# Performance work log

Hardware: AMD Instinct MI355X
Metric: run time of the kernel (lower is better)

Reference implementation:

```python
import jax, jax.numpy as jnp
import numpy as np


def _segsum(x):
    """Stable segment-sum. x: (..., l) -> (..., l, l) lower-triangular sums."""
    l = x.shape[-1]
    cs = jnp.cumsum(x, axis=-1)
    seg = cs[..., :, None] - cs[..., None, :]
    mask = jnp.tril(jnp.ones((l, l), dtype=bool))
    return jnp.where(mask, seg, -jnp.inf)


def setup_inputs() -> dict:
    key = jax.random.key(0)
    kx, ka, kb, kc = jax.random.split(key, 4)
    b, s, h, p, n = 4, 8192, 32, 64, 16
    X = jax.random.normal(kx, (b, s, h, p), dtype=jnp.float32)
    # negative A for realistic decaying SSM dynamics / numerical safety
    A = -jnp.abs(jax.random.normal(ka, (b, s, h), dtype=jnp.float32)) * 0.5
    B = jax.random.normal(kb, (b, s, h, n), dtype=jnp.float32)
    C = jax.random.normal(kc, (b, s, h, n), dtype=jnp.float32)
    return {"X": X, "A": A, "B": B, "C": C, "block_len": 64}


def reference(X, A, B, C, block_len):
    b, s, h, p = X.shape
    n = B.shape[-1]
    c = s // block_len
    l = block_len
    # chunk: (b, c, l, ...)
    Xb = X.reshape(b, c, l, h, p)
    Bb = B.reshape(b, c, l, h, n)
    Cb = C.reshape(b, c, l, h, n)
    Ab = A.reshape(b, c, l, h).transpose(0, 3, 1, 2)  # (b, h, c, l)
    A_cumsum = jnp.cumsum(Ab, axis=-1)                # (b, h, c, l)

    # 1) intra-chunk (diagonal) output
    L = jnp.exp(_segsum(Ab))                          # (b, h, c, l, l)
    Y_diag = jnp.einsum("bclhn,bcshn,bhcls,bcshp->bclhp", Cb, Bb, L, Xb)

    # 2) intra-chunk states (chunk-final state contribution)
    decay_states = jnp.exp(A_cumsum[..., -1:] - A_cumsum)   # (b, h, c, l)
    states = jnp.einsum("bclhn,bhcl,bclhp->bchpn", Bb, decay_states, Xb)

    # 3) inter-chunk recurrence (zero initial states)
    A_last = A_cumsum[..., -1]                        # (b, h, c)
    decay_chunk = jnp.exp(_segsum(jnp.pad(A_last, ((0, 0), (0, 0), (1, 0)))))  # (b,h,c+1,c+1)
    states = jnp.concatenate([jnp.zeros_like(states[:, :1]), states], axis=1)  # (b,c+1,h,p,n)
    new_states = jnp.einsum("bhzc,bchpn->bzhpn", decay_chunk, states)
    states = new_states[:, :-1]                       # states entering each chunk

    # 4) state -> output (off-diagonal)
    state_decay_out = jnp.exp(A_cumsum)               # (b, h, c, l)
    Y_off = jnp.einsum("bclhn,bchpn,bhcl->bclhp", Cb, states, state_decay_out)

    Y = (Y_diag + Y_off).reshape(b, s, h, p)
    return Y
```

## Files before the change

kernel.cpp:

```cpp
#include <hip/hip_runtime.h>

#define BB 4
#define SS 8192
#define HH 32
#define PP 64
#define NN 16
#define LL 64
#define CC 128
#define NCHAIN (BB * HH)
#define NCHT (NCHAIN * CC)

typedef __attribute__((ext_vector_type(8))) short bf16x8;
typedef __attribute__((ext_vector_type(4))) short bf16x4;
typedef __attribute__((ext_vector_type(4))) float f32x4;

__device__ inline short f2bf(float f) {
    unsigned u = __builtin_bit_cast(unsigned, f);
    u = (u + 0x7FFFu + ((u >> 16) & 1u)) >> 16;
    return (short)u;
}

__global__ __launch_bounds__(256) void k1_states(
    const float* __restrict__ X, const float* __restrict__ A,
    const float* __restrict__ B, float* __restrict__ states,
    float* __restrict__ alast_g)
{
    int blk = blockIdx.x;
    int h = blk & (HH - 1);
    int c = (blk >> 5) & (CC - 1);
    int b = blk >> 12;
    int tid = threadIdx.x;
    int w = tid >> 6, l = tid & 63, g = l >> 4, lr = l & 15;
    int chain = b * HH + h;

    __shared__ float Bs[LL][17];

    size_t row0 = (size_t)b * SS + (size_t)c * LL;
    const float* Xp = X + (row0 * HH + h) * PP;
    const float* Bp = B + (row0 * HH + h) * NN;
    const float* Ap = A + row0 * HH + h;

    float av = Ap[(size_t)l * HH];
    int r = tid >> 2, q = tid & 3;
    float4 br = *(const float4*)(Bp + (size_t)r * (HH * NN) + q * 4);
    float xr[16];
#pragma unroll
    for (int kt = 0; kt < 2; ++kt)
#pragma unroll
        for (int e = 0; e < 8; ++e)
            xr[kt * 8 + e] = Xp[(size_t)(kt * 32 + g * 8 + e) * (HH * PP) + 16 * w + lr];

    float x = av;
#pragma unroll
    for (int d = 1; d < 64; d <<= 1) {
        float t = __shfl_up(x, d, 64);
        if (l >= d) x += t;
    }
    float alast = __shfl(x, 63, 64);

    float wlr = __expf(alast - __shfl(x, r & 63, 64));
    Bs[r][q * 4 + 0] = br.x * wlr;
    Bs[r][q * 4 + 1] = br.y * wlr;
    Bs[r][q * 4 + 2] = br.z * wlr;
    Bs[r][q * 4 + 3] = br.w * wlr;
    __syncthreads();

    bf16x8 bt[2], xf[2];
#pragma unroll
    for (int kt = 0; kt < 2; ++kt)
#pragma unroll
        for (int e = 0; e < 8; ++e) {
            int row = kt * 32 + g * 8 + e;
            bt[kt][e] = f2bf(Bs[row][lr]);
            xf[kt][e] = f2bf(xr[kt * 8 + e]);
        }
    f32x4 st = __builtin_amdgcn_mfma_f32_16x16x32_bf16(bt[0], xf[0], (f32x4)0.f, 0, 0, 0);
    st = __builtin_amdgcn_mfma_f32_16x16x32_bf16(bt[1], xf[1], st, 0, 0, 0);

    float4 pv = {st[0], st[1], st[2], st[3]};
    *(float4*)(states + (size_t)(chain * CC + c) * (PP * NN) + (16 * w + lr) * NN + 4 * g) = pv;
    if (tid == 0) alast_g[chain * CC + c] = alast;
}

__global__ __launch_bounds__(256) void k2_scan(
    float* __restrict__ states, const float* __restrict__ alast_g)
{
    int chain = blockIdx.x >> 2;
    int t = ((blockIdx.x & 3) << 8) + threadIdx.x;
    __shared__ float eal[CC];
    if (threadIdx.x < CC)
        eal[threadIdx.x] = __expf(alast_g[chain * CC + threadIdx.x]);
    __syncthreads();

    float* base = states + (size_t)chain * CC * (PP * NN) + t;
    float P = 0.f;
    for (int c0 = 0; c0 < CC; c0 += 8) {
        float s[8], o[8];
#pragma unroll
        for (int u = 0; u < 8; ++u) s[u] = base[(size_t)(c0 + u) * (PP * NN)];
#pragma unroll
        for (int u = 0; u < 8; ++u) { o[u] = P; P = eal[c0 + u] * P + s[u]; }
#pragma unroll
        for (int u = 0; u < 8; ++u) base[(size_t)(c0 + u) * (PP * NN)] = o[u];
    }
}

__global__ __launch_bounds__(256) void k3_y(
    const float* __restrict__ X, const float* __restrict__ A,
    const float* __restrict__ Bm, const float* __restrict__ Cm,
    const float* __restrict__ pin, float* __restrict__ Y)
{
    int blk = blockIdx.x;
    int h = blk & (HH - 1);
    int c = (blk >> 5) & (CC - 1);
    int b = blk >> 12;
    int tid = threadIdx.x;
    int w = tid >> 6, l = tid & 63, g = l >> 4, lr = l & 15;
    int chain = b * HH + h;

    __shared__ short XTF[8 * 64 * 8];
    __shared__ short ScF[8 * 64 * 8];
    __shared__ short BsF[4 * 64 * 8];
    __shared__ short PF[4 * 64 * 8];

    size_t row0 = (size_t)b * SS + (size_t)c * LL;
    const float* Xp = X + (row0 * HH + h) * PP;
    const float* Bp = Bm + (row0 * HH + h) * NN;
    const float* Cp = Cm + (row0 * HH + h) * NN;
    const float* Ap = A + row0 * HH + h;
    float* Yp = Y + (row0 * HH + h) * PP;

    float av = Ap[(size_t)l * HH];
    int r = tid >> 2, q = tid & 3;
    float4 br = *(const float4*)(Bp + (size_t)r * (HH * NN) + q * 4);
    float4 cr0 = {0,0,0,0}, cr1 = {0,0,0,0};
    if (g < 2) {
        const float* crp = Cp + (size_t)(16 * w + lr) * (HH * NN) + g * 8;
        cr0 = *(const float4*)crp;
        cr1 = *(const float4*)(crp + 4);
    }
    float4 pinv = *(const float4*)(pin + (size_t)(chain * CC + c) * (PP * NN) + (16 * w + lr) * NN + 4 * g);
    float xr[16];
#pragma unroll
    for (int si = 0; si < 2; ++si) {
        int k0 = si * 32 + g * 8;
#pragma unroll
        for (int e = 0; e < 8; ++e)
            xr[si * 8 + e] = Xp[(size_t)(k0 + e) * (HH * PP) + 16 * w + lr];
    }

    float x = av;
#pragma unroll
    for (int d = 1; d < 64; d <<= 1) {
        float t = __shfl_up(x, d, 64);
        if (l >= d) x += t;
    }
    float cs_i[4], ei[4];
    int ib = 16 * w + 4 * g;
#pragma unroll
    for (int rr = 0; rr < 4; ++rr) {
        cs_i[rr] = __shfl(x, ib + rr, 64);
        ei[rr] = __expf(cs_i[rr]);
    }

    ((bf16x8*)ScF)[tid] = (bf16x8)0;
    ((bf16x8*)ScF)[tid + 256] = (bf16x8)0;
    if (tid < 128)
        ((bf16x8*)PF)[(tid >> 5) * 64 + 32 + (tid & 31)] = (bf16x8)0;
    {
        int fl = (r & 15) + 16 * (q >> 1);
        int jt = r >> 4;
        bf16x4 bb = { f2bf(br.x), f2bf(br.y), f2bf(br.z), f2bf(br.w) };
        ((bf16x4*)BsF)[(jt * 64 + fl) * 2 + (q & 1)] = bb;
        int zt = tid >> 6, zu = (tid >> 1) & 31, zv = tid & 1;
        ((bf16x4*)BsF)[(zt * 64 + 32 + zu) * 2 + zv] = (bf16x4)0;
    }
    {
        float P4[4] = {pinv.x, pinv.y, pinv.z, pinv.w};
#pragma unroll
        for (int rr = 0; rr < 4; ++rr) {
            int n = 4 * g + rr;
            PF[(w * 64 + (n >> 3) * 16 + lr) * 8 + (n & 7)] = f2bf(P4[rr]);
        }
    }
    bf16x8 caw = (bf16x8)0;
    if (g < 2) {
        caw[0] = f2bf(cr0.x); caw[1] = f2bf(cr0.y);
        caw[2] = f2bf(cr0.z); caw[3] = f2bf(cr0.w);
        caw[4] = f2bf(cr1.x); caw[5] = f2bf(cr1.y);
        caw[6] = f2bf(cr1.z); caw[7] = f2bf(cr1.w);
    }
    __syncthreads();

    f32x4 acc[4];
#pragma unroll
    for (int pt = 0; pt < 4; ++pt) {
        bf16x8 pfv = ((bf16x8*)PF)[pt * 64 + l];
        acc[pt] = __builtin_amdgcn_mfma_f32_16x16x32_bf16(caw, pfv, (f32x4)0.f, 0, 0, 0);
    }
#pragma unroll
    for (int pt = 0; pt < 4; ++pt)
#pragma unroll
        for (int rr = 0; rr < 4; ++rr) acc[pt][rr] *= ei[rr];

    for (int jt = 0; jt <= w; ++jt) {
        bf16x8 bw = ((bf16x8*)BsF)[jt * 64 + l];
        f32x4 sr = __builtin_amdgcn_mfma_f32_16x16x32_bf16(caw, bw, (f32x4)0.f, 0, 0, 0);
        int j = jt * 16 + lr;
        float csj = __shfl(x, j, 64);
        int kt2 = j >> 5;
        int flb = 16 * ((j >> 3) & 3);
#pragma unroll
        for (int rr = 0; rr < 4; ++rr) {
            int i15 = g * 4 + rr;
            int i = 16 * w + i15;
            float v = (j <= i) ? sr[rr] * __expf(cs_i[rr] - csj) : 0.f;
            ScF[((w * 2 + kt2) * 64 + i15 + flb) * 8 + (j & 7)] = f2bf(v);
        }
    }

#pragma unroll
    for (int si = 0; si < 2; ++si) {
        bf16x8 xb;
#pragma unroll
        for (int e = 0; e < 8; ++e) xb[e] = f2bf(xr[si * 8 + e]);
        ((bf16x8*)XTF)[tid + si * 256] = xb;
    }
    __syncthreads();

    int kts = (w >= 2) ? 2 : 1;
    for (int kt = 0; kt < kts; ++kt) {
        bf16x8 af = ((bf16x8*)ScF)[(w * 2 + kt) * 64 + l];
#pragma unroll
        for (int pt = 0; pt < 4; ++pt) {
            bf16x8 xf = ((bf16x8*)XTF)[(kt * 4 + pt) * 64 + l];
            acc[pt] = __builtin_amdgcn_mfma_f32_16x16x32_bf16(af, xf, acc[pt], 0, 0, 0);
        }
    }

#pragma unroll
    for (int pt = 0; pt < 4; ++pt)
#pragma unroll
        for (int rr = 0; rr < 4; ++rr)
            Yp[(size_t)(16 * w + 4 * g + rr) * (HH * PP) + pt * 16 + lr] = acc[pt][rr];
}

extern "C" void kernel_launch(void* const* d_in, const int* in_sizes, int n_in,
                              void* d_out, int out_size, void* d_ws, size_t ws_size,
                              hipStream_t stream)
{
    const float* X = (const float*)d_in[0];
    const float* A = (const float*)d_in[1];
    const float* B = (const float*)d_in[2];
    const float* C = (const float*)d_in[3];
    float* Y = (float*)d_out;

    float* states = (float*)d_ws;
    float* alast  = states + (size_t)NCHT * (PP * NN);

    dim3 blk(256);
    k1_states<<<dim3(NCHT), blk, 0, stream>>>(X, A, B, states, alast);
    k2_scan<<<dim3(NCHAIN * 4), blk, 0, stream>>>(states, alast);
    k3_y<<<dim3(NCHT), blk, 0, stream>>>(X, A, B, C, states, Y);
}
```

Before: 276.3 us.

## Persistent double-buffered kernels, bf16 states, and cached bf16 X fragments

The state and Y kernels become persistent: each block handles several chunks and prefetches the next chunk's inputs into registers and double-buffered shared memory while computing the current one. Chunk states are stored and scanned as bf16 instead of fp32, which halves that traffic. When the workspace is large enough, k1 also writes bf16-converted X fragments that k3 reads instead of re-reading and converting fp32 X. This trades extra workspace writes and lower state precision for less traffic and launch overhead.

Result: faster. 262.1 us (-5.2%).

```diff
diff --git a/kernel.cpp b/kernel.cpp
--- a/kernel.cpp
+++ b/kernel.cpp
@@ -9,9 +9,11 @@
 #define CC 128
 #define NCHAIN (BB * HH)
 #define NCHT (NCHAIN * CC)
+#define ITERS 8
+#define GRID1 (NCHT / ITERS)
 
 typedef __attribute__((ext_vector_type(8))) short bf16x8;
-typedef __attribute__((ext_vector_type(4))) short bf16x4;
+typedef __attribute__((ext_vector_type(4))) short s16x4;
 typedef __attribute__((ext_vector_type(4))) float f32x4;
 
 __device__ inline short f2bf(float f) {
@@ -19,11 +21,237 @@
     u = (u + 0x7FFFu + ((u >> 16) & 1u)) >> 16;
     return (short)u;
 }
+__device__ inline float bf2f(short s) {
+    unsigned u = ((unsigned)(unsigned short)s) << 16;
+    return __builtin_bit_cast(float, u);
+}
+__device__ inline float wscan(float v, int l) {
+    float x = v;
+#pragma unroll
+    for (int d = 1; d < 64; d <<= 1) {
+        float t = __shfl_up(x, d, 64);
+        if (l >= d) x += t;
+    }
+    return x;
+}
 
 __global__ __launch_bounds__(256) void k1_states(
     const float* __restrict__ X, const float* __restrict__ A,
-    const float* __restrict__ B, float* __restrict__ states,
-    float* __restrict__ alast_g)
+    const float* __restrict__ B, short* __restrict__ states,
+    float* __restrict__ alast_g, short* __restrict__ xtf, int do_xtf)
+{
+    int tid = threadIdx.x;
+    int w = tid >> 6, l = tid & 63, g = l >> 4, lr = l & 15;
+    int r = tid >> 2, q4 = tid & 3;
+    int bid = blockIdx.x;
+
+    __shared__ float Bs[2][LL][17];
+
+    float xrA[16], xrB[16];
+    float4 br; float av;
+
+#define K1_LOADS(gc_, xr_) { \
+    int h_ = (gc_) & 31, c_ = ((gc_) >> 5) & 127, b_ = (gc_) >> 12; \
+    size_t row0_ = (size_t)b_ * SS + (size_t)c_ * LL; \
+    const float* Xp_ = X + (row0_ * HH + h_) * PP; \
+    av = (A + row0_ * HH + h_)[(size_t)l * HH]; \
+    br = *(const float4*)(B + (row0_ * HH + h_) * NN + (size_t)r * (HH * NN) + q4 * 4); \
+    _Pragma("unroll") for (int kt_ = 0; kt_ < 2; ++kt_) \
+    _Pragma("unroll") for (int e_ = 0; e_ < 8; ++e_) \
+        xr_[kt_ * 8 + e_] = Xp_[(size_t)(kt_ * 32 + g * 8 + e_) * (HH * PP) + 16 * w + lr]; }
+
+#define K1_STAGE(qd_, gc_) { \
+    float x_ = wscan(av, l); \
+    float alast_ = __shfl(x_, 63, 64); \
+    float wlr_ = __expf(alast_ - __shfl(x_, r, 64)); \
+    Bs[qd_][r][q4 * 4 + 0] = br.x * wlr_; \
+    Bs[qd_][r][q4 * 4 + 1] = br.y * wlr_; \
+    Bs[qd_][r][q4 * 4 + 2] = br.z * wlr_; \
+    Bs[qd_][r][q4 * 4 + 3] = br.w * wlr_; \
+    if (tid == 0) { \
+        int h_ = (gc_) & 31, c_ = ((gc_) >> 5) & 127, b_ = (gc_) >> 12; \
+        alast_g[(b_ * HH + h_) * CC + c_] = alast_; } }
+
+#define K1_COMPUTE(qd_, xr_, gc_) { \
+    int h_ = (gc_) & 31, c_ = ((gc_) >> 5) & 127, b_ = (gc_) >> 12; \
+    size_t cc_ = (size_t)((b_ * HH + h_) * CC + c_); \
+    bf16x8 bt0_, bt1_, xf0_, xf1_; \
+    _Pragma("unroll") for (int e_ = 0; e_ < 8; ++e_) { \
+        bt0_[e_] = f2bf(Bs[qd_][g * 8 + e_][lr]); \
+        bt1_[e_] = f2bf(Bs[qd_][32 + g * 8 + e_][lr]); \
+        xf0_[e_] = f2bf(xr_[e_]); xf1_[e_] = f2bf(xr_[8 + e_]); } \
+    f32x4 st_ = __builtin_amdgcn_mfma_f32_16x16x32_bf16(bt0_, xf0_, (f32x4)0.f, 0, 0, 0); \
+    st_ = __builtin_amdgcn_mfma_f32_16x16x32_bf16(bt1_, xf1_, st_, 0, 0, 0); \
+    s16x4 sp_ = { f2bf(st_[0]), f2bf(st_[1]), f2bf(st_[2]), f2bf(st_[3]) }; \
+    *(s16x4*)(states + (cc_ << 10) + ((16 * w + lr) << 4) + (g << 2)) = sp_; \
+    if (do_xtf) { \
+        short* xd_ = xtf + (cc_ << 12); \
+        ((bf16x8*)xd_)[tid] = xf0_; \
+        ((bf16x8*)xd_)[tid + 256] = xf1_; } }
+
+    K1_LOADS(bid, xrA)
+    K1_STAGE(0, bid)
+    __syncthreads();
+#pragma unroll
+    for (int t = 0; t < ITERS; ++t) {
+        int gc_c = bid + t * GRID1;
+        int gc_n = bid + (t + 1) * GRID1;
+        if (t + 1 < ITERS) {
+            if (t & 1) { K1_LOADS(gc_n, xrA) } else { K1_LOADS(gc_n, xrB) }
+        }
+        if (t & 1) { K1_COMPUTE(t & 1, xrB, gc_c) } else { K1_COMPUTE(t & 1, xrA, gc_c) }
+        if (t + 1 < ITERS) { K1_STAGE((t & 1) ^ 1, gc_n) }
+        __syncthreads();
+    }
+#undef K1_LOADS
+#undef K1_STAGE
+#undef K1_COMPUTE
+}
+
+__global__ __launch_bounds__(256) void k2_scan(
+    short* __restrict__ states, const float* __restrict__ alast_g)
+{
+    int chain = blockIdx.x >> 2;
+    int t = ((blockIdx.x & 3) << 8) + threadIdx.x;
+    __shared__ float eal[CC];
+    if (threadIdx.x < CC)
+        eal[threadIdx.x] = __expf(alast_g[chain * CC + threadIdx.x]);
+    __syncthreads();
+
+    short* base = states + ((size_t)chain * CC << 10) + t;
+    float P = 0.f;
+    for (int c0 = 0; c0 < CC; c0 += 8) {
+        short s[8];
+#pragma unroll
+        for (int u = 0; u < 8; ++u) s[u] = base[(size_t)(c0 + u) << 10];
+#pragma unroll
+        for (int u = 0; u < 8; ++u) {
+            float o = P;
+            P = eal[c0 + u] * P + bf2f(s[u]);
+            base[(size_t)(c0 + u) << 10] = f2bf(o);
+        }
+    }
+}
+
+__global__ __launch_bounds__(256) void k3_big(
+    const float* __restrict__ A, const float* __restrict__ Bm,
+    const float* __restrict__ Cm, const short* __restrict__ pin,
+    const short* __restrict__ xtf, float* __restrict__ Y)
+{
+    int tid = threadIdx.x;
+    int w = tid >> 6, l = tid & 63, g = l >> 4, lr = l & 15;
+    int r = tid >> 2, q4 = tid & 3;
+    int bid = blockIdx.x;
+
+    __shared__ short XTF[2][8 * 64 * 8];
+    __shared__ short BsF[2][4 * 64 * 8];
+    __shared__ short PF[2][4 * 64 * 8];
+    __shared__ short ScF[8 * 64 * 8];
+
+    ((bf16x8*)ScF)[w * 128 + l] = (bf16x8)0;
+    ((bf16x8*)ScF)[w * 128 + 64 + l] = (bf16x8)0;
+    if (tid < 128) {
+        ((bf16x8*)PF[0])[(tid >> 5) * 64 + 32 + (tid & 31)] = (bf16x8)0;
+        ((bf16x8*)PF[1])[(tid >> 5) * 64 + 32 + (tid & 31)] = (bf16x8)0;
+    }
+    {
+        int zt = tid >> 6, zu = (tid >> 1) & 31, zv = tid & 1;
+        ((s16x4*)BsF[0])[(zt * 64 + 32 + zu) * 2 + zv] = (s16x4)0;
+        ((s16x4*)BsF[1])[(zt * 64 + 32 + zu) * 2 + zv] = (s16x4)0;
+    }
+
+    bf16x8 xv0, xv1, caw_c, caw_n;
+    float4 br, cr0 = {0,0,0,0}, cr1 = {0,0,0,0};
+    s16x4 pinb; float av;
+    float x_c, x_n;
+
+#define K3_LOADS(gc_) { \
+    int h_ = (gc_) & 31, c_ = ((gc_) >> 5) & 127, b_ = (gc_) >> 12; \
+    size_t row0_ = (size_t)b_ * SS + (size_t)c_ * LL; \
+    size_t cc_ = (size_t)((b_ * HH + h_) * CC + c_); \
+    const short* xs_ = xtf + (cc_ << 12); \
+    xv0 = ((const bf16x8*)xs_)[tid]; \
+    xv1 = ((const bf16x8*)xs_)[tid + 256]; \
+    av = (A + row0_ * HH + h_)[(size_t)l * HH]; \
+    br = *(const float4*)(Bm + (row0_ * HH + h_) * NN + (size_t)r * (HH * NN) + q4 * 4); \
+    if (g < 2) { \
+        const float* cp_ = Cm + (row0_ * HH + h_) * NN + (size_t)(16 * w + lr) * (HH * NN) + g * 8; \
+        cr0 = *(const float4*)cp_; cr1 = *(const float4*)(cp_ + 4); } \
+    pinb = *(const s16x4*)(pin + (cc_ << 10) + ((16 * w + lr) << 4) + (g << 2)); }
+
+#define K3_STAGE(qd_) { \
+    x_n = wscan(av, l); \
+    ((bf16x8*)XTF[qd_])[tid] = xv0; \
+    ((bf16x8*)XTF[qd_])[tid + 256] = xv1; \
+    int fl_ = (r & 15) + 16 * (q4 >> 1); \
+    int jt_ = r >> 4; \
+    s16x4 bb_ = { f2bf(br.x), f2bf(br.y), f2bf(br.z), f2bf(br.w) }; \
+    ((s16x4*)BsF[qd_])[(jt_ * 64 + fl_) * 2 + (q4 & 1)] = bb_; \
+    ((s16x4*)PF[qd_])[(w * 64 + (g >> 1) * 16 + lr) * 2 + (g & 1)] = pinb; \
+    caw_n = (bf16x8)0; \
+    if (g < 2) { \
+        caw_n[0] = f2bf(cr0.x); caw_n[1] = f2bf(cr0.y); caw_n[2] = f2bf(cr0.z); caw_n[3] = f2bf(cr0.w); \
+        caw_n[4] = f2bf(cr1.x); caw_n[5] = f2bf(cr1.y); caw_n[6] = f2bf(cr1.z); caw_n[7] = f2bf(cr1.w); } }
+
+#define K3_COMPUTE(qd_, gc_) { \
+    int h_ = (gc_) & 31, c_ = ((gc_) >> 5) & 127, b_ = (gc_) >> 12; \
+    size_t row0_ = (size_t)b_ * SS + (size_t)c_ * LL; \
+    float* Yp_ = Y + (row0_ * HH + h_) * PP; \
+    float cs_i_[4], ei_[4]; \
+    int ib_ = 16 * w + 4 * g; \
+    _Pragma("unroll") for (int rr_ = 0; rr_ < 4; ++rr_) { \
+        cs_i_[rr_] = __shfl(x_c, ib_ + rr_, 64); ei_[rr_] = __expf(cs_i_[rr_]); } \
+    f32x4 acc_[4]; \
+    _Pragma("unroll") for (int pt_ = 0; pt_ < 4; ++pt_) { \
+        bf16x8 pfv_ = ((bf16x8*)PF[qd_])[pt_ * 64 + l]; \
+        acc_[pt_] = __builtin_amdgcn_mfma_f32_16x16x32_bf16(caw_c, pfv_, (f32x4)0.f, 0, 0, 0); } \
+    _Pragma("unroll") for (int pt_ = 0; pt_ < 4; ++pt_) \
+    _Pragma("unroll") for (int rr_ = 0; rr_ < 4; ++rr_) acc_[pt_][rr_] *= ei_[rr_]; \
+    for (int jt_ = 0; jt_ <= w; ++jt_) { \
+        bf16x8 bw_ = ((bf16x8*)BsF[qd_])[jt_ * 64 + l]; \
+        f32x4 sr_ = __builtin_amdgcn_mfma_f32_16x16x32_bf16(caw_c, bw_, (f32x4)0.f, 0, 0, 0); \
+        int j_ = jt_ * 16 + lr; \
+        float csj_ = __shfl(x_c, j_, 64); \
+        int kt2_ = j_ >> 5; \
+        int flb_ = 16 * ((j_ >> 3) & 3); \
+        _Pragma("unroll") for (int rr_ = 0; rr_ < 4; ++rr_) { \
+            int i15_ = g * 4 + rr_; \
+            int i_ = 16 * w + i15_; \
+            float v_ = (j_ <= i_) ? sr_[rr_] * __expf(cs_i_[rr_] - csj_) : 0.f; \
+            ScF[((w * 2 + kt2_) * 64 + i15_ + flb_) * 8 + (j_ & 7)] = f2bf(v_); } } \
+    int kts_ = (w >= 2) ? 2 : 1; \
+    for (int kt_ = 0; kt_ < kts_; ++kt_) { \
+        bf16x8 af_ = ((bf16x8*)ScF)[(w * 2 + kt_) * 64 + l]; \
+        _Pragma("unroll") for (int pt_ = 0; pt_ < 4; ++pt_) { \
+            bf16x8 xf_ = ((bf16x8*)XTF[qd_])[(kt_ * 4 + pt_) * 64 + l]; \
+            acc_[pt_] = __builtin_amdgcn_mfma_f32_16x16x32_bf16(af_, xf_, acc_[pt_], 0, 0, 0); } } \
+    _Pragma("unroll") for (int pt_ = 0; pt_ < 4; ++pt_) \
+    _Pragma("unroll") for (int rr_ = 0; rr_ < 4; ++rr_) \
+        Yp_[(size_t)(16 * w + 4 * g + rr_) * (HH * PP) + pt_ * 16 + lr] = acc_[pt_][rr_]; }
+
+    K3_LOADS(bid)
+    K3_STAGE(0)
+    x_c = x_n; caw_c = caw_n;
+    __syncthreads();
+#pragma unroll
+    for (int t = 0; t < ITERS; ++t) {
+        if (t + 1 < ITERS) { K3_LOADS(bid + (t + 1) * GRID1) }
+        K3_COMPUTE(t & 1, bid + t * GRID1)
+        if (t + 1 < ITERS) {
+            K3_STAGE((t + 1) & 1)
+            x_c = x_n; caw_c = caw_n;
+        }
+        __syncthreads();
+    }
+#undef K3_LOADS
+#undef K3_STAGE
+#undef K3_COMPUTE
+}
+
+__global__ __launch_bounds__(256) void k3_small(
+    const float* __restrict__ X, const float* __restrict__ A,
+    const float* __restrict__ Bm, const float* __restrict__ Cm,
+    const short* __restrict__ pin, float* __restrict__ Y)
 {
     int blk = blockIdx.x;
     int h = blk & (HH - 1);
@@ -32,91 +260,7 @@
     int tid = threadIdx.x;
     int w = tid >> 6, l = tid & 63, g = l >> 4, lr = l & 15;
     int chain = b * HH + h;
-
-    __shared__ float Bs[LL][17];
-
-    size_t row0 = (size_t)b * SS + (size_t)c * LL;
-    const float* Xp = X + (row0 * HH + h) * PP;
-    const float* Bp = B + (row0 * HH + h) * NN;
-    const float* Ap = A + row0 * HH + h;
-
-    float av = Ap[(size_t)l * HH];
     int r = tid >> 2, q = tid & 3;
-    float4 br = *(const float4*)(Bp + (size_t)r * (HH * NN) + q * 4);
-    float xr[16];
-#pragma unroll
-    for (int kt = 0; kt < 2; ++kt)
-#pragma unroll
-        for (int e = 0; e < 8; ++e)
-            xr[kt * 8 + e] = Xp[(size_t)(kt * 32 + g * 8 + e) * (HH * PP) + 16 * w + lr];
-
-    float x = av;
-#pragma unroll
-    for (int d = 1; d < 64; d <<= 1) {
-        float t = __shfl_up(x, d, 64);
-        if (l >= d) x += t;
-    }
-    float alast = __shfl(x, 63, 64);
-
-    float wlr = __expf(alast - __shfl(x, r & 63, 64));
-    Bs[r][q * 4 + 0] = br.x * wlr;
-    Bs[r][q * 4 + 1] = br.y * wlr;
-    Bs[r][q * 4 + 2] = br.z * wlr;
-    Bs[r][q * 4 + 3] = br.w * wlr;
-    __syncthreads();
-
-    bf16x8 bt[2], xf[2];
-#pragma unroll
-    for (int kt = 0; kt < 2; ++kt)
-#pragma unroll
-        for (int e = 0; e < 8; ++e) {
-            int row = kt * 32 + g * 8 + e;
-            bt[kt][e] = f2bf(Bs[row][lr]);
-            xf[kt][e] = f2bf(xr[kt * 8 + e]);
-        }
-    f32x4 st = __builtin_amdgcn_mfma_f32_16x16x32_bf16(bt[0], xf[0], (f32x4)0.f, 0, 0, 0);
-    st = __builtin_amdgcn_mfma_f32_16x16x32_bf16(bt[1], xf[1], st, 0, 0, 0);
-
-    float4 pv = {st[0], st[1], st[2], st[3]};
-    *(float4*)(states + (size_t)(chain * CC + c) * (PP * NN) + (16 * w + lr) * NN + 4 * g) = pv;
-    if (tid == 0) alast_g[chain * CC + c] = alast;
-}
-
-__global__ __launch_bounds__(256) void k2_scan(
-    float* __restrict__ states, const float* __restrict__ alast_g)
-{
-    int chain = blockIdx.x >> 2;
-    int t = ((blockIdx.x & 3) << 8) + threadIdx.x;
-    __shared__ float eal[CC];
-    if (threadIdx.x < CC)
-        eal[threadIdx.x] = __expf(alast_g[chain * CC + threadIdx.x]);
-    __syncthreads();
-
-    float* base = states + (size_t)chain * CC * (PP * NN) + t;
-    float P = 0.f;
-    for (int c0 = 0; c0 < CC; c0 += 8) {
-        float s[8], o[8];
-#pragma unroll
-        for (int u = 0; u < 8; ++u) s[u] = base[(size_t)(c0 + u) * (PP * NN)];
-#pragma unroll
-        for (int u = 0; u < 8; ++u) { o[u] = P; P = eal[c0 + u] * P + s[u]; }
-#pragma unroll
-        for (int u = 0; u < 8; ++u) base[(size_t)(c0 + u) * (PP * NN)] = o[u];
-    }
-}
-
-__global__ __launch_bounds__(256) void k3_y(
-    const float* __restrict__ X, const float* __restrict__ A,
-    const float* __restrict__ Bm, const float* __restrict__ Cm,
-    const float* __restrict__ pin, float* __restrict__ Y)
-{
-    int blk = blockIdx.x;
-    int h = blk & (HH - 1);
-    int c = (blk >> 5) & (CC - 1);
-    int b = blk >> 12;
-    int tid = threadIdx.x;
-    int w = tid >> 6, l = tid & 63, g = l >> 4, lr = l & 15;
-    int chain = b * HH + h;
 
     __shared__ short XTF[8 * 64 * 8];
     __shared__ short ScF[8 * 64 * 8];
@@ -131,7 +275,6 @@
     float* Yp = Y + (row0 * HH + h) * PP;
 
     float av = Ap[(size_t)l * HH];
-    int r = tid >> 2, q = tid & 3;
     float4 br = *(const float4*)(Bp + (size_t)r * (HH * NN) + q * 4);
     float4 cr0 = {0,0,0,0}, cr1 = {0,0,0,0};
     if (g < 2) {
@@ -139,50 +282,31 @@
         cr0 = *(const float4*)crp;
         cr1 = *(const float4*)(crp + 4);
     }
-    float4 pinv = *(const float4*)(pin + (size_t)(chain * CC + c) * (PP * NN) + (16 * w + lr) * NN + 4 * g);
+    s16x4 pinb = *(const s16x4*)(pin + (((size_t)(chain * CC + c)) << 10) + ((16 * w + lr) << 4) + (g << 2));
     float xr[16];
 #pragma unroll
-    for (int si = 0; si < 2; ++si) {
-        int k0 = si * 32 + g * 8;
+    for (int si = 0; si < 2; ++si)
 #pragma unroll
         for (int e = 0; e < 8; ++e)
-            xr[si * 8 + e] = Xp[(size_t)(k0 + e) * (HH * PP) + 16 * w + lr];
-    }
-
-    float x = av;
-#pragma unroll
-    for (int d = 1; d < 64; d <<= 1) {
-        float t = __shfl_up(x, d, 64);
-        if (l >= d) x += t;
-    }
-    float cs_i[4], ei[4];
-    int ib = 16 * w + 4 * g;
-#pragma unroll
-    for (int rr = 0; rr < 4; ++rr) {
-        cs_i[rr] = __shfl(x, ib + rr, 64);
-        ei[rr] = __expf(cs_i[rr]);
-    }
-
-    ((bf16x8*)ScF)[tid] = (bf16x8)0;
-    ((bf16x8*)ScF)[tid + 256] = (bf16x8)0;
+            xr[si * 8 + e] = Xp[(size_t)(si * 32 + g * 8 + e) * (HH * PP) + 16 * w + lr];
+
+    float x = wscan(av, l);
+
+    ((bf16x8*)ScF)[w * 128 + l] = (bf16x8)0;
+    ((bf16x8*)ScF)[w * 128 + 64 + l] = (bf16x8)0;
     if (tid < 128)
         ((bf16x8*)PF)[(tid >> 5) * 64 + 32 + (tid & 31)] = (bf16x8)0;
     {
+        int zt = tid >> 6, zu = (tid >> 1) & 31, zv = tid & 1;
+        ((s16x4*)BsF)[(zt * 64 + 32 + zu) * 2 + zv] = (s16x4)0;
+    }
+    {
         int fl = (r & 15) + 16 * (q >> 1);
         int jt = r >> 4;
-        bf16x4 bb = { f2bf(br.x), f2bf(br.y), f2bf(br.z), f2bf(br.w) };
-        ((bf16x4*)BsF)[(jt * 64 + fl) * 2 + (q & 1)] = bb;
-        int zt = tid >> 6, zu = (tid >> 1) & 31, zv = tid & 1;
-        ((bf16x4*)BsF)[(zt * 64 + 32 + zu) * 2 + zv] = (bf16x4)0;
-    }
-    {
-        float P4[4] = {pinv.x, pinv.y, pinv.z, pinv.w};
-#pragma unroll
-        for (int rr = 0; rr < 4; ++rr) {
-            int n = 4 * g + rr;
-            PF[(w * 64 + (n >> 3) * 16 + lr) * 8 + (n & 7)] = f2bf(P4[rr]);
-        }
-    }
+        s16x4 bb = { f2bf(br.x), f2bf(br.y), f2bf(br.z), f2bf(br.w) };
+        ((s16x4*)BsF)[(jt * 64 + fl) * 2 + (q & 1)] = bb;
+    }
+    *(s16x4*)&PF[(w * 64 + (g >> 1) * 16 + lr) * 8 + (g & 1) * 4] = pinb;
     bf16x8 caw = (bf16x8)0;
     if (g < 2) {
         caw[0] = f2bf(cr0.x); caw[1] = f2bf(cr0.y);
@@ -191,6 +315,14 @@
         caw[6] = f2bf(cr1.z); caw[7] = f2bf(cr1.w);
     }
     __syncthreads();
+
+    float cs_i[4], ei[4];
+    int ib = 16 * w + 4 * g;
+#pragma unroll
+    for (int rr = 0; rr < 4; ++rr) {
+        cs_i[rr] = __shfl(x, ib + rr, 64);
+        ei[rr] = __expf(cs_i[rr]);
+    }
 
     f32x4 acc[4];
 #pragma unroll
@@ -255,11 +387,19 @@
     const float* C = (const float*)d_in[3];
     float* Y = (float*)d_out;
 
-    float* states = (float*)d_ws;
-    float* alast  = states + (size_t)NCHT * (PP * NN);
+    const size_t states_bytes = (size_t)NCHT * 1024 * 2;
+    const size_t alast_bytes  = (size_t)NCHT * 4;
+    const size_t xtf_bytes    = (size_t)NCHT * 4096 * 2;
+    short* states = (short*)d_ws;
+    float* alast  = (float*)((char*)d_ws + states_bytes);
+    short* xtf    = (short*)((char*)d_ws + states_bytes + alast_bytes);
+    int big = (ws_size >= states_bytes + alast_bytes + xtf_bytes) ? 1 : 0;
 
     dim3 blk(256);
-    k1_states<<<dim3(NCHT), blk, 0, stream>>>(X, A, B, states, alast);
+    k1_states<<<dim3(GRID1), blk, 0, stream>>>(X, A, B, states, alast, xtf, big);
     k2_scan<<<dim3(NCHAIN * 4), blk, 0, stream>>>(states, alast);
-    k3_y<<<dim3(NCHT), blk, 0, stream>>>(X, A, B, C, states, Y);
-}
+    if (big)
+        k3_big<<<dim3(GRID1), blk, 0, stream>>>(A, B, C, states, xtf, Y);
+    else
+        k3_small<<<dim3(NCHT), blk, 0, stream>>>(X, A, B, C, states, Y);
+}
```
